# Performance work log

Hardware: AMD Instinct MI355X
Metric: run time of the kernel (lower is better)

The kernel has to match this reference:

```python
import jax, jax.numpy as jnp
import numpy as np

NC, NZ = 128, 256
H_IN = W_IN = 64
UK = US = 8          # unfold kernel == stride (non-overlapping patches)
CS = 2               # conv stride
CK, CP = 4, 1        # conv kernel / padding
HP = H_IN // US      # 8 patch rows
WP = W_IN // US      # 8 patch cols
OK = UK // CS        # 4 = per-patch conv output size
BN_EPS = 1e-5
LRELU = 0.2


def setup_inputs() -> dict:
    key = jax.random.key(0)
    k1, k2, k3, k4 = jax.random.split(key, 4)
    B = 32
    input = jax.random.normal(k1, (B, NC, H_IN, W_IN), dtype=jnp.float32)
    # grouped (locally-connected) conv weight: [H*W*nz, nc, ck, ck]
    weight = jax.random.normal(k2, (HP * WP * NZ, NC, CK, CK), dtype=jnp.float32) * 0.05
    gamma = jax.random.uniform(k3, (HP * WP * NZ,), dtype=jnp.float32)
    beta = jax.random.normal(k4, (HP * WP * NZ,), dtype=jnp.float32) * 0.1
    return {"input": input, "weight": weight, "gamma": gamma, "beta": beta}


def reference(input, weight, gamma, beta):
    B = input.shape[0]
    # --- Unfold (non-overlapping 8x8 patches), matching reshape/permute in torch ---
    # [B, nc, H, uk, W, uk] -> [B, H, W, nc, uk, uk] -> [B, H*W*nc, uk, uk]
    x = input.reshape(B, NC, HP, UK, WP, UK)
    x = x.transpose(0, 2, 4, 1, 3, 5).reshape(B, HP * WP * NC, UK, UK)
    # --- Grouped conv: groups = H*W, each group nc -> nz, 4x4 k, stride 2, pad 1 ---
    y = jax.lax.conv_general_dilated(
        x, weight, window_strides=(CS, CS), padding=((CP, CP), (CP, CP)),
        feature_group_count=HP * WP)  # [B, H*W*nz, ok, ok]
    # --- BatchNorm2d (training mode: batch stats, biased variance) ---
    mean = jnp.mean(y, axis=(0, 2, 3))
    var = jnp.var(y, axis=(0, 2, 3))
    inv = gamma / jnp.sqrt(var + BN_EPS)
    y = y * inv[None, :, None, None] + (beta - mean * inv)[None, :, None, None]
    # --- LeakyReLU(0.2) ---
    y = jnp.where(y > 0, y, LRELU * y)
    # --- Fold (kernel == stride == 4 -> pure block reassembly) ---
    # [B, H, W, nz, ok, ok] -> [B, nz, H, ok, W, ok] -> [B, nz, hlatent, wlatent]
    y = y.reshape(B, HP, WP, NZ, OK, OK)
    out = y.transpose(0, 3, 1, 4, 2, 5).reshape(B, NZ, HP * OK, WP * OK)
    return out
```

## Files before the change

### kernel.cpp

```cpp
#include <hip/hip_runtime.h>

namespace {
constexpr float kLrelu = 0.2f;
constexpr float kEps   = 1e-5f;
}

typedef short bf16x8 __attribute__((ext_vector_type(8)));
typedef float f32x4  __attribute__((ext_vector_type(4)));

#define LDS_BARRIER() asm volatile("s_waitcnt lgkmcnt(0)\n\ts_barrier" ::: "memory")

static __device__ __forceinline__ unsigned f2bf(float x) {
  unsigned u = __float_as_uint(x);
  return (u + 0x7FFFu + ((u >> 16) & 1u)) >> 16;
}
static __device__ __forceinline__ unsigned packbf(float a, float b) {
  return f2bf(a) | (f2bf(b) << 16);
}

__global__ __launch_bounds__(512, 4) void conv_bn_fused(
    const float* __restrict__ input,
    const float* __restrict__ weight,
    float* __restrict__ out,
    const float* __restrict__ gamma,
    const float* __restrict__ beta)
{
  __shared__ __align__(16) float raw0[64 * 64];
  __shared__ __align__(16) float raw1[64 * 64];
  __shared__ __align__(16) char Bs[512 * 64];
  __shared__ __align__(16) char As[64 * 64];

  const int bid  = blockIdx.x;
  const int orig = (bid & 7) * 32 + (bid >> 3);
  const int g    = orig >> 2;
  const int zt   = orig & 3;
  const int hp = g >> 3, wp = g & 7;
  const int z0 = zt * 64;

  const int tid  = threadIdx.x;
  const int lane = tid & 63;
  const int w    = tid >> 6;
  const int llo  = lane & 15, lhi = lane >> 4;

  const int pl_s  = tid >> 3;
  const int f4    = tid & 7;
  const int bl_s  = pl_s >> 1;
  const int ncs_s = pl_s & 1;
  const int py_s  = f4 >> 1, h_s = f4 & 1;
  const float* const gsrc = input
      + ((size_t)bl_s * 128 + ncs_s) * 4096
      + (hp * 8 + py_s) * 64 + wp * 8 + (h_s << 2);
  const int roffA = pl_s * 64 + ((py_s ^ (bl_s & 7)) << 3) + (h_s << 2);
  const int roffB = pl_s * 64 + (((py_s + 4) ^ (bl_s & 7)) << 3) + (h_s << 2);
  float* const rd0a = raw0 + roffA;  float* const rd0b = raw0 + roffB;
  float* const rd1a = raw1 + roffA;  float* const rd1b = raw1 + roffB;

  const int az0 = tid >> 3;
  const int kq  = tid & 7;
  const float* const wsrc =
      weight + ((size_t)(g * 256 + z0 + az0)) * 2048 + kq * 4;
  const int aswz = (az0 >> 1) & 3;
  char* const ad0 = As + az0 * 64 + (((kq >> 1) ^ aswz) << 4) + ((kq & 1) << 3);

  const int bl_g = tid >> 4;
  const int oy_g = (tid >> 2) & 3;
  const int ky_g = tid & 3;
  const int iy   = 2 * oy_g - 1 + ky_g;
  const unsigned rowm = ((unsigned)iy < 8u) ? 0xFFFFFFFFu : 0u;
  const int iyc  = iy < 0 ? 0 : (iy > 7 ? 7 : iy);
  const int swzg = bl_g & 7;
  const int gro0 = (bl_g * 2 + 0) * 64 + ((iyc ^ swzg) << 3);
  const int gro1 = (bl_g * 2 + 1) * 64 + ((iyc ^ swzg) << 3);
  char* bwd[2][4];
#pragma unroll
  for (int ncs = 0; ncs < 2; ++ncs)
#pragma unroll
    for (int ox = 0; ox < 4; ++ox) {
      const int ml = bl_g * 16 + oy_g * 4 + ox;
      const int gk = ncs * 2 + (ky_g >> 1);
      bwd[ncs][ox] = Bs + ml * 64 + ((gk ^ ((ml >> 1) & 3)) << 4) + ((ky_g & 1) << 3);
    }

  const char* afp[4];
#pragma unroll
  for (int zf = 0; zf < 4; ++zf) {
    const int ar = zf * 16 + llo;
    afp[zf] = As + ar * 64 + ((lhi ^ ((ar >> 1) & 3)) << 4);
  }
  const char* bfp[4];
#pragma unroll
  for (int mf = 0; mf < 4; ++mf) {
    const int mr = w * 64 + mf * 16 + llo;
    bfp[mf] = Bs + mr * 64 + ((lhi ^ ((mr >> 1) & 3)) << 4);
  }

  f32x4 acc[4][4] = {};

  uint2 ub[2][4];
  auto gather = [&](const float* rw) {
#pragma unroll
    for (int ncs = 0; ncs < 2; ++ncs) {
      const int gro = ncs ? gro1 : gro0;
      const float4 r0 = *(const float4*)(rw + gro);
      const float4 r1 = *(const float4*)(rw + gro + 4);
      uint2 t;
      t.x = packbf(0.f, r0.x) & rowm;  t.y = packbf(r0.y, r0.z) & rowm;  ub[ncs][0] = t;
      t.x = packbf(r0.y, r0.z) & rowm; t.y = packbf(r0.w, r1.x) & rowm;  ub[ncs][1] = t;
      t.x = packbf(r0.w, r1.x) & rowm; t.y = packbf(r1.y, r1.z) & rowm;  ub[ncs][2] = t;
      t.x = packbf(r1.y, r1.z) & rowm; t.y = packbf(r1.w, 0.f) & rowm;   ub[ncs][3] = t;
    }
  };
  auto writeB = [&]() {
#pragma unroll
    for (int ncs = 0; ncs < 2; ++ncs)
#pragma unroll
      for (int ox = 0; ox < 4; ++ox) *(uint2*)bwd[ncs][ox] = ub[ncs][ox];
  };
  auto domfma = [&]() {
    bf16x8 bfv[4];
#pragma unroll
    for (int mf = 0; mf < 4; ++mf) bfv[mf] = *(const bf16x8*)bfp[mf];
#pragma unroll
    for (int zf = 0; zf < 4; ++zf) {
      const bf16x8 af = *(const bf16x8*)afp[zf];
#pragma unroll
      for (int mf = 0; mf < 4; ++mf)
        acc[zf][mf] = __builtin_amdgcn_mfma_f32_16x16x32_bf16(af, bfv[mf], acc[zf][mf], 0, 0, 0);
    }
  };

  float4 ra0 = *(const float4*)(gsrc);
  float4 ra1 = *(const float4*)(gsrc + 256);
  float4 rb0 = *(const float4*)(gsrc + 8192);
  float4 rb1 = *(const float4*)(gsrc + 8192 + 256);
  float4 wa  = *(const float4*)(wsrc);
  float4 wb  = *(const float4*)(wsrc + 32);
  *(float4*)rd0a = ra0;
  *(float4*)rd0b = ra1;
  LDS_BARRIER();

  for (int ck = 0; ck < 64; ck += 2) {
    {
      uint2 a0w;
      a0w.x = packbf(wa.x, wa.y); a0w.y = packbf(wa.z, wa.w);
      if (ck + 2 < 64) {
        ra0 = *(const float4*)(gsrc + (size_t)(ck + 2) * 8192);
        ra1 = *(const float4*)(gsrc + (size_t)(ck + 2) * 8192 + 256);
        wa  = *(const float4*)(wsrc + (ck + 2) * 32);
      }
      gather(raw0);
      LDS_BARRIER();
      *(uint2*)ad0 = a0w;
      writeB();
      *(float4*)rd1a = rb0;
      *(float4*)rd1b = rb1;
      LDS_BARRIER();
      domfma();
    }
    {
      uint2 a0w;
      a0w.x = packbf(wb.x, wb.y); a0w.y = packbf(wb.z, wb.w);
      if (ck + 3 < 64) {
        rb0 = *(const float4*)(gsrc + (size_t)(ck + 3) * 8192);
        rb1 = *(const float4*)(gsrc + (size_t)(ck + 3) * 8192 + 256);
        wb  = *(const float4*)(wsrc + (ck + 3) * 32);
      }
      gather(raw1);
      LDS_BARRIER();
      *(uint2*)ad0 = a0w;
      writeB();
      if (ck + 2 < 64) { *(float4*)rd0a = ra0; *(float4*)rd0b = ra1; }
      LDS_BARRIER();
      domfma();
    }
  }

  __syncthreads();
  float* const sums  = (float*)raw0;
  float* const sums2 = sums + 512;
#pragma unroll
  for (int zf = 0; zf < 4; ++zf) {
    float s[4], ss[4];
#pragma unroll
    for (int r = 0; r < 4; ++r) {
      s[r]  = acc[zf][0][r] + acc[zf][1][r] + acc[zf][2][r] + acc[zf][3][r];
      ss[r] = acc[zf][0][r] * acc[zf][0][r] + acc[zf][1][r] * acc[zf][1][r]
            + acc[zf][2][r] * acc[zf][2][r] + acc[zf][3][r] * acc[zf][3][r];
    }
#pragma unroll
    for (int off = 1; off <= 8; off <<= 1) {
#pragma unroll
      for (int r = 0; r < 4; ++r) {
        s[r]  += __shfl_xor(s[r], off);
        ss[r] += __shfl_xor(ss[r], off);
      }
    }
    if (llo == 0) {
#pragma unroll
      for (int r = 0; r < 4; ++r) {
        const int chl = zf * 16 + lhi * 4 + r;
        sums[chl * 8 + w]  = s[r];
        sums2[chl * 8 + w] = ss[r];
      }
    }
  }
  __syncthreads();
  float* const invL = (float*)raw1;
  float* const shL  = invL + 64;
  if (tid < 64) {
    float sum = 0.f, sq = 0.f;
#pragma unroll
    for (int i = 0; i < 8; ++i) { sum += sums[tid * 8 + i]; sq += sums2[tid * 8 + i]; }
    const int ch = g * 256 + z0 + tid;
    const float mean = sum * (1.f / 512.f);
    const float var  = fmaf(-mean, mean, sq * (1.f / 512.f));
    const float iv   = gamma[ch] * rsqrtf(var + kEps);
    invL[tid] = iv;
    shL[tid]  = fmaf(-mean, iv, beta[ch]);
  }
  __syncthreads();

#pragma unroll
  for (int zf = 0; zf < 4; ++zf) {
    float iv[4], sh[4];
#pragma unroll
    for (int r = 0; r < 4; ++r) {
      const int chl = zf * 16 + lhi * 4 + r;
      iv[r] = invL[chl];
      sh[r] = shL[chl];
    }
    const int zch = z0 + zf * 16 + lhi * 4;
#pragma unroll
    for (int mf = 0; mf < 4; ++mf) {
      const int mm  = w * 64 + mf * 16 + llo;
      const int bb  = mm >> 4;
      const int o_y = (mm >> 2) & 3;
      const int o_x = mm & 3;
      float* op = out + (((size_t)bb * 256 + zch) * 32 + hp * 4 + o_y) * 32
                      + wp * 4 + o_x;
#pragma unroll
      for (int r = 0; r < 4; ++r) {
        float y = fmaf(acc[zf][mf][r], iv[r], sh[r]);
        y = y > 0.f ? y : kLrelu * y;
        op[(size_t)r * 1024] = y;
      }
    }
  }
}

extern "C" void kernel_launch(void* const* d_in, const int* in_sizes, int n_in,
                              void* d_out, int out_size, void* d_ws, size_t ws_size,
                              hipStream_t stream) {
  const float* input  = (const float*)d_in[0];
  const float* weight = (const float*)d_in[1];
  const float* gamma  = (const float*)d_in[2];
  const float* beta   = (const float*)d_in[3];
  float* out = (float*)d_out;

  conv_bn_fused<<<256, 512, 0, stream>>>(input, weight, out, gamma, beta);
}
```

Baseline: 89.76 us.

## Build im2col tiles directly from global rows, dropping raw LDS staging

Each thread now loads one full 8-wide input patch row straight from global memory, packs it to bf16 in registers, and scatters it into the two B-tile positions that row feeds. This removes the raw0/raw1 LDS staging buffers and the LDS read-back gather step. Out-of-range conv taps are handled with a zero mask on the second write. Launch bounds go from 4 to 2 blocks per SM, freeing registers, and the BN reduction scratch now reuses the Bs buffer. Cutting 32 KB of LDS per block may also let more blocks fit per CU.

```diff
diff --git a/kernel.cpp b/kernel.cpp
--- a/kernel.cpp
+++ b/kernel.cpp
@@ -18,15 +18,13 @@
   return f2bf(a) | (f2bf(b) << 16);
 }
 
-__global__ __launch_bounds__(512, 4) void conv_bn_fused(
+__global__ __launch_bounds__(512, 2) void conv_bn_fused(
     const float* __restrict__ input,
     const float* __restrict__ weight,
     float* __restrict__ out,
     const float* __restrict__ gamma,
     const float* __restrict__ beta)
 {
-  __shared__ __align__(16) float raw0[64 * 64];
-  __shared__ __align__(16) float raw1[64 * 64];
   __shared__ __align__(16) char Bs[512 * 64];
   __shared__ __align__(16) char As[64 * 64];
 
@@ -43,17 +41,31 @@
   const int llo  = lane & 15, lhi = lane >> 4;
 
   const int pl_s  = tid >> 3;
-  const int f4    = tid & 7;
+  const int py_s  = tid & 7;
   const int bl_s  = pl_s >> 1;
   const int ncs_s = pl_s & 1;
-  const int py_s  = f4 >> 1, h_s = f4 & 1;
   const float* const gsrc = input
       + ((size_t)bl_s * 128 + ncs_s) * 4096
-      + (hp * 8 + py_s) * 64 + wp * 8 + (h_s << 2);
-  const int roffA = pl_s * 64 + ((py_s ^ (bl_s & 7)) << 3) + (h_s << 2);
-  const int roffB = pl_s * 64 + (((py_s + 4) ^ (bl_s & 7)) << 3) + (h_s << 2);
-  float* const rd0a = raw0 + roffA;  float* const rd0b = raw0 + roffB;
-  float* const rd1a = raw1 + roffA;  float* const rd1b = raw1 + roffB;
+      + (hp * 8 + py_s) * 64 + wp * 8;
+
+  const int oy1 = (py_s + 1) >> 1 > 3 ? 3 : (py_s + 1) >> 1;
+  const int ky1 = py_s + 1 - 2 * oy1;
+  const bool z2 = (py_s == 0) || (py_s == 7);
+  const int oy2 = py_s == 0 ? 0 : (py_s == 7 ? 3 : oy1 - 1);
+  const int ky2 = py_s == 0 ? 0 : (py_s == 7 ? 3 : ky1 + 2);
+  const unsigned m2 = z2 ? 0u : 0xFFFFFFFFu;
+
+  char* bwd1[4];
+  char* bwd2[4];
+#pragma unroll
+  for (int ox = 0; ox < 4; ++ox) {
+    const int ml1 = bl_s * 16 + oy1 * 4 + ox;
+    const int gk1 = ncs_s * 2 + (ky1 >> 1);
+    bwd1[ox] = Bs + ml1 * 64 + ((gk1 ^ ((ml1 >> 1) & 3)) << 4) + ((ky1 & 1) << 3);
+    const int ml2 = bl_s * 16 + oy2 * 4 + ox;
+    const int gk2 = ncs_s * 2 + (ky2 >> 1);
+    bwd2[ox] = Bs + ml2 * 64 + ((gk2 ^ ((ml2 >> 1) & 3)) << 4) + ((ky2 & 1) << 3);
+  }
 
   const int az0 = tid >> 3;
   const int kq  = tid & 7;
@@ -62,25 +74,6 @@
   const int aswz = (az0 >> 1) & 3;
   char* const ad0 = As + az0 * 64 + (((kq >> 1) ^ aswz) << 4) + ((kq & 1) << 3);
 
-  const int bl_g = tid >> 4;
-  const int oy_g = (tid >> 2) & 3;
-  const int ky_g = tid & 3;
-  const int iy   = 2 * oy_g - 1 + ky_g;
-  const unsigned rowm = ((unsigned)iy < 8u) ? 0xFFFFFFFFu : 0u;
-  const int iyc  = iy < 0 ? 0 : (iy > 7 ? 7 : iy);
-  const int swzg = bl_g & 7;
-  const int gro0 = (bl_g * 2 + 0) * 64 + ((iyc ^ swzg) << 3);
-  const int gro1 = (bl_g * 2 + 1) * 64 + ((iyc ^ swzg) << 3);
-  char* bwd[2][4];
-#pragma unroll
-  for (int ncs = 0; ncs < 2; ++ncs)
-#pragma unroll
-    for (int ox = 0; ox < 4; ++ox) {
-      const int ml = bl_g * 16 + oy_g * 4 + ox;
-      const int gk = ncs * 2 + (ky_g >> 1);
-      bwd[ncs][ox] = Bs + ml * 64 + ((gk ^ ((ml >> 1) & 3)) << 4) + ((ky_g & 1) << 3);
-    }
-
   const char* afp[4];
 #pragma unroll
   for (int zf = 0; zf < 4; ++zf) {
@@ -96,25 +89,16 @@
 
   f32x4 acc[4][4] = {};
 
-  uint2 ub[2][4];
-  auto gather = [&](const float* rw) {
-#pragma unroll
-    for (int ncs = 0; ncs < 2; ++ncs) {
-      const int gro = ncs ? gro1 : gro0;
-      const float4 r0 = *(const float4*)(rw + gro);
-      const float4 r1 = *(const float4*)(rw + gro + 4);
-      uint2 t;
-      t.x = packbf(0.f, r0.x) & rowm;  t.y = packbf(r0.y, r0.z) & rowm;  ub[ncs][0] = t;
-      t.x = packbf(r0.y, r0.z) & rowm; t.y = packbf(r0.w, r1.x) & rowm;  ub[ncs][1] = t;
-      t.x = packbf(r0.w, r1.x) & rowm; t.y = packbf(r1.y, r1.z) & rowm;  ub[ncs][2] = t;
-      t.x = packbf(r1.y, r1.z) & rowm; t.y = packbf(r1.w, 0.f) & rowm;   ub[ncs][3] = t;
-    }
+  unsigned pk[5];
+  auto packRow = [&](const float4& q0, const float4& q1) {
+    pk[0] = packbf(0.f, q0.x);
+    pk[1] = packbf(q0.y, q0.z);
+    pk[2] = packbf(q0.w, q1.x);
+    pk[3] = packbf(q1.y, q1.z);
+    pk[4] = packbf(q1.w, 0.f);
   };
-  auto writeB = [&]() {
-#pragma unroll
-    for (int ncs = 0; ncs < 2; ++ncs)
-#pragma unroll
-      for (int ox = 0; ox < 4; ++ox) *(uint2*)bwd[ncs][ox] = ub[ncs][ox];
+  auto writeTiles = [&](unsigned aw) {
+    *(uint2*)ad0 = *(uint2*)&aw;
   };
   auto domfma = [&]() {
     bf16x8 bfv[4];
@@ -129,55 +113,63 @@
     }
   };
 
-  float4 ra0 = *(const float4*)(gsrc);
-  float4 ra1 = *(const float4*)(gsrc + 256);
-  float4 rb0 = *(const float4*)(gsrc + 8192);
-  float4 rb1 = *(const float4*)(gsrc + 8192 + 256);
-  float4 wa  = *(const float4*)(wsrc);
-  float4 wb  = *(const float4*)(wsrc + 32);
-  *(float4*)rd0a = ra0;
-  *(float4*)rd0b = ra1;
-  LDS_BARRIER();
+  float4 rA0 = *(const float4*)(gsrc);
+  float4 rA1 = *(const float4*)(gsrc + 4);
+  float4 rB0 = *(const float4*)(gsrc + 8192);
+  float4 rB1 = *(const float4*)(gsrc + 8192 + 4);
+  float4 wA  = *(const float4*)(wsrc);
+  float4 wB  = *(const float4*)(wsrc + 32);
 
   for (int ck = 0; ck < 64; ck += 2) {
     {
+      packRow(rA0, rA1);
       uint2 a0w;
-      a0w.x = packbf(wa.x, wa.y); a0w.y = packbf(wa.z, wa.w);
+      a0w.x = packbf(wA.x, wA.y); a0w.y = packbf(wA.z, wA.w);
       if (ck + 2 < 64) {
-        ra0 = *(const float4*)(gsrc + (size_t)(ck + 2) * 8192);
-        ra1 = *(const float4*)(gsrc + (size_t)(ck + 2) * 8192 + 256);
-        wa  = *(const float4*)(wsrc + (ck + 2) * 32);
-      }
-      gather(raw0);
+        rA0 = *(const float4*)(gsrc + (size_t)(ck + 2) * 8192);
+        rA1 = *(const float4*)(gsrc + (size_t)(ck + 2) * 8192 + 4);
+        wA  = *(const float4*)(wsrc + (ck + 2) * 32);
+      }
       LDS_BARRIER();
       *(uint2*)ad0 = a0w;
-      writeB();
-      *(float4*)rd1a = rb0;
-      *(float4*)rd1b = rb1;
+#pragma unroll
+      for (int ox = 0; ox < 4; ++ox) {
+        uint2 t1; t1.x = pk[ox]; t1.y = pk[ox + 1];
+        *(uint2*)bwd1[ox] = t1;
+        uint2 t2; t2.x = pk[ox] & m2; t2.y = pk[ox + 1] & m2;
+        *(uint2*)bwd2[ox] = t2;
+      }
       LDS_BARRIER();
       domfma();
     }
     {
+      packRow(rB0, rB1);
       uint2 a0w;
-      a0w.x = packbf(wb.x, wb.y); a0w.y = packbf(wb.z, wb.w);
+      a0w.x = packbf(wB.x, wB.y); a0w.y = packbf(wB.z, wB.w);
       if (ck + 3 < 64) {
-        rb0 = *(const float4*)(gsrc + (size_t)(ck + 3) * 8192);
-        rb1 = *(const float4*)(gsrc + (size_t)(ck + 3) * 8192 + 256);
-        wb  = *(const float4*)(wsrc + (ck + 3) * 32);
-      }
-      gather(raw1);
+        rB0 = *(const float4*)(gsrc + (size_t)(ck + 3) * 8192);
+        rB1 = *(const float4*)(gsrc + (size_t)(ck + 3) * 8192 + 4);
+        wB  = *(const float4*)(wsrc + (ck + 3) * 32);
+      }
       LDS_BARRIER();
       *(uint2*)ad0 = a0w;
-      writeB();
-      if (ck + 2 < 64) { *(float4*)rd0a = ra0; *(float4*)rd0b = ra1; }
+#pragma unroll
+      for (int ox = 0; ox < 4; ++ox) {
+        uint2 t1; t1.x = pk[ox]; t1.y = pk[ox + 1];
+        *(uint2*)bwd1[ox] = t1;
+        uint2 t2; t2.x = pk[ox] & m2; t2.y = pk[ox + 1] & m2;
+        *(uint2*)bwd2[ox] = t2;
+      }
       LDS_BARRIER();
       domfma();
     }
   }
 
   __syncthreads();
-  float* const sums  = (float*)raw0;
+  float* const sums  = (float*)Bs;
   float* const sums2 = sums + 512;
+  float* const invL  = sums2 + 512;
+  float* const shL   = invL + 64;
 #pragma unroll
   for (int zf = 0; zf < 4; ++zf) {
     float s[4], ss[4];
@@ -205,8 +197,6 @@
     }
   }
   __syncthreads();
-  float* const invL = (float*)raw1;
-  float* const shL  = invL + 64;
   if (tid < 64) {
     float sum = 0.f, sq = 0.f;
 #pragma unroll
```

Result: slower. 114.1 us (+27.1%).

## Make conv main loop wave-private to drop block-wide LDS barriers

Applied to the files above, without the earlier changes.

Each wave now stages and gathers only its own batch slice of input into a private LDS region, so the per-channel block barriers in the main loop are removed. Weight fragments are loaded directly from global memory into registers in MFMA A layout instead of going through shared LDS. The cost is that every wave reloads the same weight data (8x redundant global/L2 traffic), and occupancy is lowered by the larger 64KB LDS allocation and the launch bound change from 4 to 2.

```diff
diff --git a/kernel.cpp b/kernel.cpp
--- a/kernel.cpp
+++ b/kernel.cpp
@@ -8,7 +8,7 @@
 typedef short bf16x8 __attribute__((ext_vector_type(8)));
 typedef float f32x4  __attribute__((ext_vector_type(4)));
 
-#define LDS_BARRIER() asm volatile("s_waitcnt lgkmcnt(0)\n\ts_barrier" ::: "memory")
+union U4BF8 { uint4 u; bf16x8 v; };
 
 static __device__ __forceinline__ unsigned f2bf(float x) {
   unsigned u = __float_as_uint(x);
@@ -18,17 +18,14 @@
   return f2bf(a) | (f2bf(b) << 16);
 }
 
-__global__ __launch_bounds__(512, 4) void conv_bn_fused(
+__global__ __launch_bounds__(512, 2) void conv_bn_fused(
     const float* __restrict__ input,
     const float* __restrict__ weight,
     float* __restrict__ out,
     const float* __restrict__ gamma,
     const float* __restrict__ beta)
 {
-  __shared__ __align__(16) float raw0[64 * 64];
-  __shared__ __align__(16) float raw1[64 * 64];
-  __shared__ __align__(16) char Bs[512 * 64];
-  __shared__ __align__(16) char As[64 * 64];
+  __shared__ __align__(16) char lds[65536];
 
   const int bid  = blockIdx.x;
   const int orig = (bid & 7) * 32 + (bid >> 3);
@@ -42,56 +39,54 @@
   const int w    = tid >> 6;
   const int llo  = lane & 15, lhi = lane >> 4;
 
-  const int pl_s  = tid >> 3;
-  const int f4    = tid & 7;
-  const int bl_s  = pl_s >> 1;
-  const int ncs_s = pl_s & 1;
-  const int py_s  = f4 >> 1, h_s = f4 & 1;
-  const float* const gsrc = input
-      + ((size_t)bl_s * 128 + ncs_s) * 4096
-      + (hp * 8 + py_s) * 64 + wp * 8 + (h_s << 2);
-  const int roffA = pl_s * 64 + ((py_s ^ (bl_s & 7)) << 3) + (h_s << 2);
-  const int roffB = pl_s * 64 + (((py_s + 4) ^ (bl_s & 7)) << 3) + (h_s << 2);
-  float* const rd0a = raw0 + roffA;  float* const rd0b = raw0 + roffB;
-  float* const rd1a = raw1 + roffA;  float* const rd1b = raw1 + roffB;
-
-  const int az0 = tid >> 3;
-  const int kq  = tid & 7;
-  const float* const wsrc =
-      weight + ((size_t)(g * 256 + z0 + az0)) * 2048 + kq * 4;
-  const int aswz = (az0 >> 1) & 3;
-  char* const ad0 = As + az0 * 64 + (((kq >> 1) ^ aswz) << 4) + ((kq & 1) << 3);
-
-  const int bl_g = tid >> 4;
-  const int oy_g = (tid >> 2) & 3;
-  const int ky_g = tid & 3;
+  char*  const BsW   = lds + w * 4096;
+  float* const rawW0 = (float*)(lds + 32768 + w * 4096);
+  float* const rawW1 = rawW0 + 512;
+
+  const float* sPtrG[2];
+  int sOffL[2];
+#pragma unroll
+  for (int t = 0; t < 2; ++t) {
+    const int i  = t * 64 + lane;
+    const int pl = i >> 4;
+    const int q  = i & 15;
+    const int py = q >> 1, h = q & 1;
+    const int bl = w * 4 + (pl >> 1);
+    const int nc = pl & 1;
+    sPtrG[t] = input + ((size_t)bl * 128 + nc) * 4096
+             + (hp * 8 + py) * 64 + wp * 8 + (h << 2);
+    sOffL[t] = pl * 64 + ((py ^ (bl & 7)) << 3) + (h << 2);
+  }
+
+  const float* wfp[4];
+#pragma unroll
+  for (int zf = 0; zf < 4; ++zf)
+    wfp[zf] = weight + ((size_t)(g * 256 + z0 + zf * 16 + llo)) * 2048 + lhi * 8;
+
+  const int bl_r = lane >> 4;
+  const int oy_g = (lane >> 2) & 3;
+  const int ky_g = lane & 3;
+  const int blg  = w * 4 + bl_r;
   const int iy   = 2 * oy_g - 1 + ky_g;
   const unsigned rowm = ((unsigned)iy < 8u) ? 0xFFFFFFFFu : 0u;
   const int iyc  = iy < 0 ? 0 : (iy > 7 ? 7 : iy);
-  const int swzg = bl_g & 7;
-  const int gro0 = (bl_g * 2 + 0) * 64 + ((iyc ^ swzg) << 3);
-  const int gro1 = (bl_g * 2 + 1) * 64 + ((iyc ^ swzg) << 3);
+  const int gro0 = (bl_r * 2 + 0) * 64 + ((iyc ^ (blg & 7)) << 3);
+  const int gro1 = gro0 + 64;
   char* bwd[2][4];
 #pragma unroll
   for (int ncs = 0; ncs < 2; ++ncs)
 #pragma unroll
     for (int ox = 0; ox < 4; ++ox) {
-      const int ml = bl_g * 16 + oy_g * 4 + ox;
-      const int gk = ncs * 2 + (ky_g >> 1);
-      bwd[ncs][ox] = Bs + ml * 64 + ((gk ^ ((ml >> 1) & 3)) << 4) + ((ky_g & 1) << 3);
-    }
-
-  const char* afp[4];
-#pragma unroll
-  for (int zf = 0; zf < 4; ++zf) {
-    const int ar = zf * 16 + llo;
-    afp[zf] = As + ar * 64 + ((lhi ^ ((ar >> 1) & 3)) << 4);
-  }
+      const int mlw = bl_r * 16 + oy_g * 4 + ox;
+      const int gk  = ncs * 2 + (ky_g >> 1);
+      bwd[ncs][ox] = BsW + mlw * 64 + ((gk ^ ((mlw >> 1) & 3)) << 4) + ((ky_g & 1) << 3);
+    }
+
   const char* bfp[4];
 #pragma unroll
   for (int mf = 0; mf < 4; ++mf) {
-    const int mr = w * 64 + mf * 16 + llo;
-    bfp[mf] = Bs + mr * 64 + ((lhi ^ ((mr >> 1) & 3)) << 4);
+    const int mr = mf * 16 + llo;
+    bfp[mf] = BsW + mr * 64 + ((lhi ^ ((mr >> 1) & 3)) << 4);
   }
 
   f32x4 acc[4][4] = {};
@@ -116,68 +111,60 @@
 #pragma unroll
       for (int ox = 0; ox < 4; ++ox) *(uint2*)bwd[ncs][ox] = ub[ncs][ox];
   };
-  auto domfma = [&]() {
+
+  float4 r0t0 = *(const float4*)(sPtrG[0]);
+  float4 r0t1 = *(const float4*)(sPtrG[1]);
+  *(float4*)(rawW0 + sOffL[0]) = r0t0;
+  *(float4*)(rawW0 + sOffL[1]) = r0t1;
+  float4 rrA = *(const float4*)(sPtrG[0] + 8192);
+  float4 rrB = *(const float4*)(sPtrG[1] + 8192);
+
+  for (int ck = 0; ck < 64; ++ck) {
+    float4 av[8];
+#pragma unroll
+    for (int zf = 0; zf < 4; ++zf) {
+      av[2 * zf]     = *(const float4*)(wfp[zf] + ck * 32);
+      av[2 * zf + 1] = *(const float4*)(wfp[zf] + ck * 32 + 4);
+    }
+    float4 rnA, rnB;
+    if (ck + 2 < 64) {
+      rnA = *(const float4*)(sPtrG[0] + (size_t)(ck + 2) * 8192);
+      rnB = *(const float4*)(sPtrG[1] + (size_t)(ck + 2) * 8192);
+    }
+    if (ck + 1 < 64) {
+      float* dst = ((ck + 1) & 1) ? rawW1 : rawW0;
+      *(float4*)(dst + sOffL[0]) = rrA;
+      *(float4*)(dst + sOffL[1]) = rrB;
+    }
+    gather((ck & 1) ? rawW1 : rawW0);
+    writeB();
+    bf16x8 afv[4];
+#pragma unroll
+    for (int zf = 0; zf < 4; ++zf) {
+      U4BF8 c;
+      c.u.x = packbf(av[2 * zf].x,     av[2 * zf].y);
+      c.u.y = packbf(av[2 * zf].z,     av[2 * zf].w);
+      c.u.z = packbf(av[2 * zf + 1].x, av[2 * zf + 1].y);
+      c.u.w = packbf(av[2 * zf + 1].z, av[2 * zf + 1].w);
+      afv[zf] = c.v;
+    }
     bf16x8 bfv[4];
 #pragma unroll
     for (int mf = 0; mf < 4; ++mf) bfv[mf] = *(const bf16x8*)bfp[mf];
 #pragma unroll
-    for (int zf = 0; zf < 4; ++zf) {
-      const bf16x8 af = *(const bf16x8*)afp[zf];
+    for (int zf = 0; zf < 4; ++zf)
 #pragma unroll
       for (int mf = 0; mf < 4; ++mf)
-        acc[zf][mf] = __builtin_amdgcn_mfma_f32_16x16x32_bf16(af, bfv[mf], acc[zf][mf], 0, 0, 0);
-    }
-  };
-
-  float4 ra0 = *(const float4*)(gsrc);
-  float4 ra1 = *(const float4*)(gsrc + 256);
-  float4 rb0 = *(const float4*)(gsrc + 8192);
-  float4 rb1 = *(const float4*)(gsrc + 8192 + 256);
-  float4 wa  = *(const float4*)(wsrc);
-  float4 wb  = *(const float4*)(wsrc + 32);
-  *(float4*)rd0a = ra0;
-  *(float4*)rd0b = ra1;
-  LDS_BARRIER();
-
-  for (int ck = 0; ck < 64; ck += 2) {
-    {
-      uint2 a0w;
-      a0w.x = packbf(wa.x, wa.y); a0w.y = packbf(wa.z, wa.w);
-      if (ck + 2 < 64) {
-        ra0 = *(const float4*)(gsrc + (size_t)(ck + 2) * 8192);
-        ra1 = *(const float4*)(gsrc + (size_t)(ck + 2) * 8192 + 256);
-        wa  = *(const float4*)(wsrc + (ck + 2) * 32);
-      }
-      gather(raw0);
-      LDS_BARRIER();
-      *(uint2*)ad0 = a0w;
-      writeB();
-      *(float4*)rd1a = rb0;
-      *(float4*)rd1b = rb1;
-      LDS_BARRIER();
-      domfma();
-    }
-    {
-      uint2 a0w;
-      a0w.x = packbf(wb.x, wb.y); a0w.y = packbf(wb.z, wb.w);
-      if (ck + 3 < 64) {
-        rb0 = *(const float4*)(gsrc + (size_t)(ck + 3) * 8192);
-        rb1 = *(const float4*)(gsrc + (size_t)(ck + 3) * 8192 + 256);
-        wb  = *(const float4*)(wsrc + (ck + 3) * 32);
-      }
-      gather(raw1);
-      LDS_BARRIER();
-      *(uint2*)ad0 = a0w;
-      writeB();
-      if (ck + 2 < 64) { *(float4*)rd0a = ra0; *(float4*)rd0b = ra1; }
-      LDS_BARRIER();
-      domfma();
-    }
+        acc[zf][mf] = __builtin_amdgcn_mfma_f32_16x16x32_bf16(afv[zf], bfv[mf], acc[zf][mf], 0, 0, 0);
+    rrA = rnA;
+    rrB = rnB;
   }
 
   __syncthreads();
-  float* const sums  = (float*)raw0;
+  float* const sums  = (float*)lds;
   float* const sums2 = sums + 512;
+  float* const invL  = sums2 + 512;
+  float* const shL   = invL + 64;
 #pragma unroll
   for (int zf = 0; zf < 4; ++zf) {
     float s[4], ss[4];
@@ -205,8 +192,6 @@
     }
   }
   __syncthreads();
-  float* const invL = (float*)raw1;
-  float* const shL  = invL + 64;
   if (tid < 64) {
     float sum = 0.f, sq = 0.f;
 #pragma unroll
```

New measurement: 154.7 us. 72.4% more time.
